# Performance work log

Hardware: AMD Instinct MI355X
Metric: run time of the kernel (lower is better)

## Reference

```python
import jax, jax.numpy as jnp
import numpy as np

GROUPS = 8

def conv1d(x, w, b, stride=1, groups=1):
    # x: [B,C,L], w: [O, I//groups, K]
    y = jax.lax.conv_general_dilated(x, w, (stride,), 'VALID',
        dimension_numbers=('NCH', 'OIH', 'NCH'), feature_group_count=groups)
    return y + b[None, :, None]

def shuffle1d(x, groups):
    B, C, L = x.shape
    cpg = C // groups
    return x.reshape(B, groups, cpg, L).transpose(0, 2, 1, 3).reshape(B, C, L)

def setup_inputs() -> dict:
    key = jax.random.key(0)
    ks = jax.random.split(key, 12)
    C = 256
    B, L = 8, 4096
    g = GROUPS
    sc = 0.05
    inp = {
        'x':   jax.random.normal(ks[0], (B, C, L), dtype=jnp.float32),
        'w1':  jax.random.normal(ks[1], (C, C // g, 3), dtype=jnp.float32) * sc,
        'b1':  jax.random.normal(ks[2], (C,), dtype=jnp.float32) * sc,
        'w2':  jax.random.normal(ks[3], (C, C // g, 3), dtype=jnp.float32) * sc,
        'b2':  jax.random.normal(ks[4], (C,), dtype=jnp.float32) * sc,
        'wa1': jax.random.normal(ks[5], (C, 2 * C // g, 1), dtype=jnp.float32) * sc,
        'ba1': jax.random.normal(ks[6], (C,), dtype=jnp.float32) * sc,
        'wa2': jax.random.normal(ks[7], (C, C // g, 1), dtype=jnp.float32) * sc,
        'ba2': jax.random.normal(ks[8], (C,), dtype=jnp.float32) * sc,
        'w3':  jax.random.normal(ks[9], (C, C // g, 5), dtype=jnp.float32) * sc,  # kernel_size-4=5
        'b3':  jax.random.normal(ks[10], (C,), dtype=jnp.float32) * sc,
    }
    return inp

def reference(x, w1, b1, w2, b2, wa1, ba1, wa2, ba2, w3, b3):
    g = GROUPS
    # in_state has length 0 at init, so cat is identity; L >= kernel_size.
    h = conv1d(x, w1, b1, stride=1, groups=g)      # [B,C,L-2]
    h = shuffle1d(h, g)
    h = conv1d(h, w2, b2, stride=1, groups=g)      # [B,C,L-4]
    h = shuffle1d(h, g)
    # SortAttn: stable ascending sort over channel dim
    sorted_h = jnp.sort(h, axis=1, stable=True)
    a = conv1d(jnp.concatenate((sorted_h, h), axis=1), wa1, ba1, stride=1, groups=g)
    a = shuffle1d(a, g)
    a = jax.nn.sigmoid(conv1d(a, wa2, ba2, stride=1, groups=g))
    h = h * a
    y = conv1d(h, w3, b3, stride=1, groups=g)      # [B,C,L-8]
    return y
```

## Files before the change

### kernel.cpp

```cpp
#include <hip/hip_runtime.h>
#include <math.h>

#define BB 8
#define CCH 256
#define LLEN 4096
#define L1V 4094
#define L2V 4092
#define L3V 4088
#define NCOL (BB * L2V)

__global__ void prep_kernel(const float* __restrict__ wa1, const float* __restrict__ wa2,
                            float* __restrict__ wt1T, float* __restrict__ wt2T) {
    int i = blockIdx.x;
    int o = threadIdx.x;
    if (i < 64) {
        wt1T[i * 256 + o] = wa1[o * 64 + i];
    } else {
        int ii = i - 64;
        if (ii < 32) wt2T[ii * 256 + o] = wa2[o * 32 + ii];
    }
}

__global__ __launch_bounds__(256, 4) void conv1_kernel(const float* __restrict__ x,
                                                       const float* __restrict__ w1,
                                                       const float* __restrict__ b1,
                                                       float* __restrict__ t1) {
    __shared__ float xs[9248];
    const int b = blockIdx.y;
    const int l0 = blockIdx.x * 32;
    const int t = threadIdx.x;

#pragma unroll
    for (int j = 0; j < 9; ++j) {
        int f = t + 256 * j;
        int row = f / 9;
        int q = f - row * 9;
        size_t rb = (size_t)(b * CCH + row) * LLEN;
        float4 v;
        int base = l0 + 4 * q;
        if (base + 3 < LLEN) {
            v = *(const float4*)(x + rb + base);
        } else {
            v.x = x[rb + min(base + 0, LLEN - 1)];
            v.y = x[rb + min(base + 1, LLEN - 1)];
            v.z = x[rb + min(base + 2, LLEN - 1)];
            v.w = x[rb + min(base + 3, LLEN - 1)];
        }
        int a = row * 36 + (row >> 5) * 4 + 4 * q;
        *(float4*)&xs[a] = v;
    }
    __syncthreads();

    const int oc = t;
    const int go = t >> 5;
    float acc[32];
#pragma unroll
    for (int l = 0; l < 32; ++l) acc[l] = 0.f;

    for (int i = 0; i < 32; ++i) {
        int row = go * 32 + i;
        int base = row * 36 + go * 4;
        float wv0 = w1[oc * 96 + i * 3 + 0];
        float wv1 = w1[oc * 96 + i * 3 + 1];
        float wv2 = w1[oc * 96 + i * 3 + 2];
#pragma unroll
        for (int q = 0; q < 9; ++q) {
            float4 v = *(const float4*)&xs[base + 4 * q];
#pragma unroll
            for (int j = 0; j < 4; ++j) {
                int e = 4 * q + j;
                float xv = (&v.x)[j];
                if (e < 32) acc[e] += wv0 * xv;
                if (e >= 1 && e <= 32) acc[e - 1] += wv1 * xv;
                if (e >= 2 && e <= 33) acc[e - 2] += wv2 * xv;
            }
        }
    }
    float bias = b1[oc];
    int nc = (oc & 31) * 8 + (oc >> 5);
    float* dst = t1 + (size_t)(b * L1V + l0) * CCH + nc;
#pragma unroll
    for (int l = 0; l < 32; ++l) {
        if (l0 + l < L1V) dst[(size_t)l * CCH] = acc[l] + bias;
    }
}

__global__ __launch_bounds__(256, 4) void conv2_kernel(const float* __restrict__ t1,
                                                       const float* __restrict__ w2,
                                                       const float* __restrict__ b2,
                                                       float* __restrict__ t2) {
    __shared__ float ts[9792];
    const int b = blockIdx.y;
    const int l0 = blockIdx.x * 32;
    const int t = threadIdx.x;

#pragma unroll
    for (int j = 0; j < 9; ++j) {
        int f = t + 256 * j;
        if (f < 2176) {
            int p = f >> 6;
            int c4 = (f & 63) * 4;
            int row = min(l0 + p, L1V - 1);
            float4 v = *(const float4*)(t1 + (size_t)(b * L1V + row) * CCH + c4);
            *(float4*)&ts[p * 288 + (c4 >> 5) * 36 + (c4 & 31)] = v;
        }
    }
    __syncthreads();

    const int oc = t;
    const int go = t >> 5;
    float acc[32];
#pragma unroll
    for (int l = 0; l < 32; ++l) acc[l] = 0.f;

    for (int i4 = 0; i4 < 8; ++i4) {
        float wv[12];
#pragma unroll
        for (int z = 0; z < 12; ++z) wv[z] = w2[oc * 96 + i4 * 12 + z];
        int colbase = go * 36 + i4 * 4;
#pragma unroll
        for (int p = 0; p < 34; ++p) {
            float4 rv = *(const float4*)&ts[p * 288 + colbase];
#pragma unroll
            for (int cc = 0; cc < 4; ++cc) {
                float xv = (&rv.x)[cc];
#pragma unroll
                for (int k = 0; k < 3; ++k) {
                    int l = p - k;
                    if (l >= 0 && l < 32) acc[l] += wv[cc * 3 + k] * xv;
                }
            }
        }
    }
    float bias = b2[oc];
    int nc = (oc & 31) * 8 + (oc >> 5);
    float* dst = t2 + (size_t)(b * L2V + l0) * CCH + nc;
#pragma unroll
    for (int l = 0; l < 32; ++l) {
        if (l0 + l < L2V) dst[(size_t)l * CCH] = acc[l] + bias;
    }
}

__device__ __forceinline__ void ce_pair(float& a, float& b, bool up) {
    float lo = fminf(a, b), hi = fmaxf(a, b);
    a = up ? lo : hi;
    b = up ? hi : lo;
}

__device__ __forceinline__ void bitonic256(float v[4], int lane) {
#pragma unroll
    for (int k = 2; k <= 256; k <<= 1) {
#pragma unroll
        for (int j = k >> 1; j > 0; j >>= 1) {
            if (j >= 4) {
                int lm = j >> 2;
                bool upper = (lane & lm) != 0;
#pragma unroll
                for (int r = 0; r < 4; ++r) {
                    float other = __shfl_xor(v[r], lm, 64);
                    bool dirUp = (((4 * lane + r) & k) == 0);
                    bool keepMin = (dirUp != upper);
                    float lo = fminf(v[r], other), hi = fmaxf(v[r], other);
                    v[r] = keepMin ? lo : hi;
                }
            } else if (j == 2) {
#pragma unroll
                for (int r = 0; r < 2; ++r) {
                    bool up = (((4 * lane + r) & k) == 0);
                    ce_pair(v[r], v[r + 2], up);
                }
            } else {
#pragma unroll
                for (int r = 0; r < 4; r += 2) {
                    bool up = (((4 * lane + r) & k) == 0);
                    ce_pair(v[r], v[r + 1], up);
                }
            }
        }
    }
}

__global__ __launch_bounds__(256, 4) void attn_kernel(float* __restrict__ t2,
                                                      const float* __restrict__ wt1T,
                                                      const float* __restrict__ wt2T,
                                                      const float* __restrict__ ba1,
                                                      const float* __restrict__ ba2) {
    __shared__ float sm[8320];
    const int t = threadIdx.x;
    const int wv = t >> 6;
    const int lane = t & 63;
    const int wbase = wv * 2080;
    const int go = lane >> 3;

    float4 ba1v = *(const float4*)&ba1[4 * lane];
    float4 ba2v = *(const float4*)&ba2[4 * lane];

    const int colBase = blockIdx.x * 16 + wv * 4;

    float4 hv[4];
#pragma unroll
    for (int cc = 0; cc < 4; ++cc) {
        hv[cc] = *(const float4*)(t2 + (size_t)(colBase + cc) * CCH + 4 * lane);
    }
#pragma unroll
    for (int r = 0; r < 4; ++r) {
        int e = 4 * lane + r;
        int slot = ((e >> 6) + 4) * 65 + (e & 63);
        float4 vvv = make_float4((&hv[0].x)[r], (&hv[1].x)[r], (&hv[2].x)[r], (&hv[3].x)[r]);
        *(float4*)&sm[wbase + slot * 4] = vvv;
    }
    float srt[4][4];
#pragma unroll
    for (int cc = 0; cc < 4; ++cc) {
        float s[4] = {hv[cc].x, hv[cc].y, hv[cc].z, hv[cc].w};
        bitonic256(s, lane);
        srt[cc][0] = s[0]; srt[cc][1] = s[1]; srt[cc][2] = s[2]; srt[cc][3] = s[3];
    }
#pragma unroll
    for (int r = 0; r < 4; ++r) {
        int e = 4 * lane + r;
        int slot = (e >> 6) * 65 + (e & 63);
        float4 vvv = make_float4(srt[0][r], srt[1][r], srt[2][r], srt[3][r]);
        *(float4*)&sm[wbase + slot * 4] = vvv;
    }

    float4 acc[4];
#pragma unroll
    for (int cc = 0; cc < 4; ++cc) acc[cc] = make_float4(0.f, 0.f, 0.f, 0.f);
#pragma unroll 4
    for (int i = 0; i < 64; ++i) {
        float4 w4 = *(const float4*)&wt1T[i * 256 + 4 * lane];
        float4 cv = *(const float4*)&sm[wbase + (go * 65 + i) * 4];
#pragma unroll
        for (int cc = 0; cc < 4; ++cc) {
            float cvv = (&cv.x)[cc];
            acc[cc].x += w4.x * cvv;
            acc[cc].y += w4.y * cvv;
            acc[cc].z += w4.z * cvv;
            acc[cc].w += w4.w * cvv;
        }
    }
#pragma unroll
    for (int r = 0; r < 4; ++r) {
        float bb = (&ba1v.x)[r];
        float4 vvv = make_float4((&acc[0].x)[r] + bb, (&acc[1].x)[r] + bb,
                                 (&acc[2].x)[r] + bb, (&acc[3].x)[r] + bb);
        *(float4*)&sm[wbase + (5 * lane + r) * 4] = vvv;
    }

    float4 acc2[4];
#pragma unroll
    for (int cc = 0; cc < 4; ++cc) acc2[cc] = make_float4(0.f, 0.f, 0.f, 0.f);
#pragma unroll 4
    for (int i = 0; i < 32; ++i) {
        float4 w4 = *(const float4*)&wt2T[i * 256 + 4 * lane];
        int idx = ((i & 7) << 5) + (go << 2) + (i >> 3);
        int slotA = idx + (idx >> 2);
        float4 av = *(const float4*)&sm[wbase + slotA * 4];
#pragma unroll
        for (int cc = 0; cc < 4; ++cc) {
            float avv = (&av.x)[cc];
            acc2[cc].x += w4.x * avv;
            acc2[cc].y += w4.y * avv;
            acc2[cc].z += w4.z * avv;
            acc2[cc].w += w4.w * avv;
        }
    }
#pragma unroll
    for (int cc = 0; cc < 4; ++cc) {
        float zx = acc2[cc].x + ba2v.x;
        float zy = acc2[cc].y + ba2v.y;
        float zz = acc2[cc].z + ba2v.z;
        float zw = acc2[cc].w + ba2v.w;
        float4 res;
        res.x = hv[cc].x * (1.f / (1.f + __expf(-zx)));
        res.y = hv[cc].y * (1.f / (1.f + __expf(-zy)));
        res.z = hv[cc].z * (1.f / (1.f + __expf(-zz)));
        res.w = hv[cc].w * (1.f / (1.f + __expf(-zw)));
        *(float4*)(t2 + (size_t)(colBase + cc) * CCH + 4 * lane) = res;
    }
}

__global__ __launch_bounds__(256, 4) void conv3_kernel(const float* __restrict__ hm,
                                                       const float* __restrict__ w3,
                                                       const float* __restrict__ b3,
                                                       float* __restrict__ out) {
    __shared__ float ts[10368];
    const int b = blockIdx.y;
    const int l0 = blockIdx.x * 32;
    const int t = threadIdx.x;

#pragma unroll
    for (int j = 0; j < 9; ++j) {
        int f = t + 256 * j;
        int p = f >> 6;
        int c4 = (f & 63) * 4;
        int row = min(l0 + p, L2V - 1);
        float4 v = *(const float4*)(hm + (size_t)(b * L2V + row) * CCH + c4);
        *(float4*)&ts[p * 288 + (c4 >> 5) * 36 + (c4 & 31)] = v;
    }
    __syncthreads();

    const int oc = t;
    const int go = t >> 5;
    float acc[32];
#pragma unroll
    for (int l = 0; l < 32; ++l) acc[l] = 0.f;

    for (int i4 = 0; i4 < 8; ++i4) {
        float wv[20];
#pragma unroll
        for (int z = 0; z < 20; ++z) wv[z] = w3[oc * 160 + i4 * 20 + z];
        int colbase = go * 36 + i4 * 4;
#pragma unroll
        for (int p = 0; p < 36; ++p) {
            float4 rv = *(const float4*)&ts[p * 288 + colbase];
#pragma unroll
            for (int cc = 0; cc < 4; ++cc) {
                float xv = (&rv.x)[cc];
#pragma unroll
                for (int k = 0; k < 5; ++k) {
                    int l = p - k;
                    if (l >= 0 && l < 32) acc[l] += wv[cc * 5 + k] * xv;
                }
            }
        }
    }
    float bias = b3[oc];
    float* dst = out + (size_t)(b * CCH + oc) * L3V + l0;
#pragma unroll
    for (int l4 = 0; l4 < 8; ++l4) {
        int gl = l0 + 4 * l4;
        if (gl + 3 < L3V) {
            float4 v;
            v.x = acc[4 * l4 + 0] + bias;
            v.y = acc[4 * l4 + 1] + bias;
            v.z = acc[4 * l4 + 2] + bias;
            v.w = acc[4 * l4 + 3] + bias;
            *(float4*)(dst + 4 * l4) = v;
        } else {
#pragma unroll
            for (int c = 0; c < 4; ++c) {
                if (gl + c < L3V) dst[4 * l4 + c] = acc[4 * l4 + c] + bias;
            }
        }
    }
}

extern "C" void kernel_launch(void* const* d_in, const int* in_sizes, int n_in,
                              void* d_out, int out_size, void* d_ws, size_t ws_size,
                              hipStream_t stream) {
    const float* x   = (const float*)d_in[0];
    const float* w1  = (const float*)d_in[1];
    const float* b1  = (const float*)d_in[2];
    const float* w2  = (const float*)d_in[3];
    const float* b2  = (const float*)d_in[4];
    const float* wa1 = (const float*)d_in[5];
    const float* ba1 = (const float*)d_in[6];
    const float* wa2 = (const float*)d_in[7];
    const float* ba2 = (const float*)d_in[8];
    const float* w3  = (const float*)d_in[9];
    const float* b3  = (const float*)d_in[10];
    float* out = (float*)d_out;

    char* ws = (char*)d_ws;
    float* t1   = (float*)ws;
    float* t2   = (float*)(ws + ((size_t)32 << 20));
    float* wt1T = (float*)(ws + ((size_t)64 << 20));
    float* wt2T = wt1T + 64 * 256;

    hipLaunchKernelGGL(prep_kernel, dim3(96), dim3(256), 0, stream, wa1, wa2, wt1T, wt2T);
    hipLaunchKernelGGL(conv1_kernel, dim3(128, BB), dim3(256), 0, stream, x, w1, b1, t1);
    hipLaunchKernelGGL(conv2_kernel, dim3(128, BB), dim3(256), 0, stream, t1, w2, b2, t2);
    hipLaunchKernelGGL(attn_kernel, dim3(2046), dim3(256), 0, stream, t2, wt1T, wt2T, ba1, ba2);
    hipLaunchKernelGGL(conv3_kernel, dim3(128, BB), dim3(256), 0, stream, t2, w3, b3, out);
}
```

Before: 303.2 us.

## Transpose conv weights, interleave bitonic sorts with swizzles, XOR-swizzle attn smem

The prep kernel now also transposes w1, w2 and w3 so that the per-output-channel weight loads in the three conv kernels are coalesced across threads instead of strided. The attention kernel's bitonic sort is rewritten as compile-time templates that sort all four columns together, using ds_swizzle for intra-32 lane exchanges and interleaving the independent columns for ILP. Its shared-memory padding is replaced by an XOR swizzle, which shrinks LDS and raises launch bounds to 5 blocks. This risks more register pressure from sorting 16 values at once under the tighter occupancy bound.

```diff
diff --git a/kernel.cpp b/kernel.cpp
--- a/kernel.cpp
+++ b/kernel.cpp
@@ -10,19 +10,28 @@
 #define NCOL (BB * L2V)
 
 __global__ void prep_kernel(const float* __restrict__ wa1, const float* __restrict__ wa2,
-                            float* __restrict__ wt1T, float* __restrict__ wt2T) {
-    int i = blockIdx.x;
+                            const float* __restrict__ w1, const float* __restrict__ w2,
+                            const float* __restrict__ w3,
+                            float* __restrict__ wt1T, float* __restrict__ wt2T,
+                            float* __restrict__ w1T, float* __restrict__ w2T,
+                            float* __restrict__ w3T) {
+    int r = blockIdx.x;
     int o = threadIdx.x;
-    if (i < 64) {
-        wt1T[i * 256 + o] = wa1[o * 64 + i];
+    if (r < 64) {
+        wt1T[r * 256 + o] = wa1[o * 64 + r];
+    } else if (r < 96) {
+        wt2T[(r - 64) * 256 + o] = wa2[o * 32 + (r - 64)];
+    } else if (r < 192) {
+        w1T[(r - 96) * 256 + o] = w1[o * 96 + (r - 96)];
+    } else if (r < 288) {
+        w2T[(r - 192) * 256 + o] = w2[o * 96 + (r - 192)];
     } else {
-        int ii = i - 64;
-        if (ii < 32) wt2T[ii * 256 + o] = wa2[o * 32 + ii];
+        w3T[(r - 288) * 256 + o] = w3[o * 160 + (r - 288)];
     }
 }
 
 __global__ __launch_bounds__(256, 4) void conv1_kernel(const float* __restrict__ x,
-                                                       const float* __restrict__ w1,
+                                                       const float* __restrict__ w1T,
                                                        const float* __restrict__ b1,
                                                        float* __restrict__ t1) {
     __shared__ float xs[9248];
@@ -60,9 +69,9 @@
     for (int i = 0; i < 32; ++i) {
         int row = go * 32 + i;
         int base = row * 36 + go * 4;
-        float wv0 = w1[oc * 96 + i * 3 + 0];
-        float wv1 = w1[oc * 96 + i * 3 + 1];
-        float wv2 = w1[oc * 96 + i * 3 + 2];
+        float wv0 = w1T[(i * 3 + 0) * 256 + oc];
+        float wv1 = w1T[(i * 3 + 1) * 256 + oc];
+        float wv2 = w1T[(i * 3 + 2) * 256 + oc];
 #pragma unroll
         for (int q = 0; q < 9; ++q) {
             float4 v = *(const float4*)&xs[base + 4 * q];
@@ -86,7 +95,7 @@
 }
 
 __global__ __launch_bounds__(256, 4) void conv2_kernel(const float* __restrict__ t1,
-                                                       const float* __restrict__ w2,
+                                                       const float* __restrict__ w2T,
                                                        const float* __restrict__ b2,
                                                        float* __restrict__ t2) {
     __shared__ float ts[9792];
@@ -116,7 +125,7 @@
     for (int i4 = 0; i4 < 8; ++i4) {
         float wv[12];
 #pragma unroll
-        for (int z = 0; z < 12; ++z) wv[z] = w2[oc * 96 + i4 * 12 + z];
+        for (int z = 0; z < 12; ++z) wv[z] = w2T[(i4 * 12 + z) * 256 + oc];
         int colbase = go * 36 + i4 * 4;
 #pragma unroll
         for (int p = 0; p < 34; ++p) {
@@ -147,49 +156,63 @@
     b = up ? hi : lo;
 }
 
-__device__ __forceinline__ void bitonic256(float v[4], int lane) {
-#pragma unroll
-    for (int k = 2; k <= 256; k <<= 1) {
-#pragma unroll
-        for (int j = k >> 1; j > 0; j >>= 1) {
-            if (j >= 4) {
-                int lm = j >> 2;
-                bool upper = (lane & lm) != 0;
-#pragma unroll
-                for (int r = 0; r < 4; ++r) {
-                    float other = __shfl_xor(v[r], lm, 64);
-                    bool dirUp = (((4 * lane + r) & k) == 0);
-                    bool keepMin = (dirUp != upper);
-                    float lo = fminf(v[r], other), hi = fmaxf(v[r], other);
-                    v[r] = keepMin ? lo : hi;
-                }
-            } else if (j == 2) {
-#pragma unroll
-                for (int r = 0; r < 2; ++r) {
-                    bool up = (((4 * lane + r) & k) == 0);
-                    ce_pair(v[r], v[r + 2], up);
-                }
-            } else {
-#pragma unroll
-                for (int r = 0; r < 4; r += 2) {
-                    bool up = (((4 * lane + r) & k) == 0);
-                    ce_pair(v[r], v[r + 1], up);
-                }
+template<int LM>
+__device__ __forceinline__ float swz(float x) {
+    return __int_as_float(__builtin_amdgcn_ds_swizzle(__float_as_int(x), (LM << 10) | 0x1F));
+}
+
+template<int K, int J>
+__device__ __forceinline__ void mstep(float v[4][4], int lane) {
+    if constexpr (J >= 4) {
+        constexpr int LM = J >> 2;
+        const bool upper = (lane & LM) != 0;
+#pragma unroll
+        for (int r = 0; r < 4; ++r) {
+            const bool dirUp = (((4 * lane + r) & K) == 0);
+            const bool keepMin = (dirUp != upper);
+#pragma unroll
+            for (int c = 0; c < 4; ++c) {
+                float other;
+                if constexpr (LM == 32) other = __shfl_xor(v[c][r], 32, 64);
+                else other = swz<LM>(v[c][r]);
+                float lo = fminf(v[c][r], other), hi = fmaxf(v[c][r], other);
+                v[c][r] = keepMin ? lo : hi;
             }
         }
-    }
-}
-
-__global__ __launch_bounds__(256, 4) void attn_kernel(float* __restrict__ t2,
+    } else if constexpr (J == 2) {
+#pragma unroll
+        for (int r = 0; r < 2; ++r) {
+            const bool up = (((4 * lane + r) & K) == 0);
+#pragma unroll
+            for (int c = 0; c < 4; ++c) ce_pair(v[c][r], v[c][r + 2], up);
+        }
+    } else {
+#pragma unroll
+        for (int r = 0; r < 4; r += 2) {
+            const bool up = (((4 * lane + r) & K) == 0);
+#pragma unroll
+            for (int c = 0; c < 4; ++c) ce_pair(v[c][r], v[c][r + 1], up);
+        }
+    }
+    if constexpr (J > 1) mstep<K, (J >> 1)>(v, lane);
+}
+
+template<int K>
+__device__ __forceinline__ void msort(float v[4][4], int lane) {
+    mstep<K, (K >> 1)>(v, lane);
+    if constexpr (K < 256) msort<(K << 1)>(v, lane);
+}
+
+__global__ __launch_bounds__(256, 5) void attn_kernel(float* __restrict__ t2,
                                                       const float* __restrict__ wt1T,
                                                       const float* __restrict__ wt2T,
                                                       const float* __restrict__ ba1,
                                                       const float* __restrict__ ba2) {
-    __shared__ float sm[8320];
+    __shared__ float sm[8192];
     const int t = threadIdx.x;
     const int wv = t >> 6;
     const int lane = t & 63;
-    const int wbase = wv * 2080;
+    const int wbase = wv << 11;
     const int go = lane >> 3;
 
     float4 ba1v = *(const float4*)&ba1[4 * lane];
@@ -205,22 +228,24 @@
 #pragma unroll
     for (int r = 0; r < 4; ++r) {
         int e = 4 * lane + r;
-        int slot = ((e >> 6) + 4) * 65 + (e & 63);
+        int ch = (e >> 6) + 4;
+        int slot = ch * 64 + ((e & 63) ^ ch);
         float4 vvv = make_float4((&hv[0].x)[r], (&hv[1].x)[r], (&hv[2].x)[r], (&hv[3].x)[r]);
         *(float4*)&sm[wbase + slot * 4] = vvv;
     }
-    float srt[4][4];
-#pragma unroll
-    for (int cc = 0; cc < 4; ++cc) {
-        float s[4] = {hv[cc].x, hv[cc].y, hv[cc].z, hv[cc].w};
-        bitonic256(s, lane);
-        srt[cc][0] = s[0]; srt[cc][1] = s[1]; srt[cc][2] = s[2]; srt[cc][3] = s[3];
-    }
+    float v[4][4];
+#pragma unroll
+    for (int cc = 0; cc < 4; ++cc)
+#pragma unroll
+        for (int r = 0; r < 4; ++r) v[cc][r] = (&hv[cc].x)[r];
+    msort<2>(v, lane);
+
 #pragma unroll
     for (int r = 0; r < 4; ++r) {
         int e = 4 * lane + r;
-        int slot = (e >> 6) * 65 + (e & 63);
-        float4 vvv = make_float4(srt[0][r], srt[1][r], srt[2][r], srt[3][r]);
+        int ch = e >> 6;
+        int slot = ch * 64 + ((e & 63) ^ ch);
+        float4 vvv = make_float4(v[0][r], v[1][r], v[2][r], v[3][r]);
         *(float4*)&sm[wbase + slot * 4] = vvv;
     }
 
@@ -230,7 +255,7 @@
 #pragma unroll 4
     for (int i = 0; i < 64; ++i) {
         float4 w4 = *(const float4*)&wt1T[i * 256 + 4 * lane];
-        float4 cv = *(const float4*)&sm[wbase + (go * 65 + i) * 4];
+        float4 cv = *(const float4*)&sm[wbase + (go * 64 + (i ^ go)) * 4];
 #pragma unroll
         for (int cc = 0; cc < 4; ++cc) {
             float cvv = (&cv.x)[cc];
@@ -282,7 +307,7 @@
 }
 
 __global__ __launch_bounds__(256, 4) void conv3_kernel(const float* __restrict__ hm,
-                                                       const float* __restrict__ w3,
+                                                       const float* __restrict__ w3T,
                                                        const float* __restrict__ b3,
                                                        float* __restrict__ out) {
     __shared__ float ts[10368];
@@ -310,7 +335,7 @@
     for (int i4 = 0; i4 < 8; ++i4) {
         float wv[20];
 #pragma unroll
-        for (int z = 0; z < 20; ++z) wv[z] = w3[oc * 160 + i4 * 20 + z];
+        for (int z = 0; z < 20; ++z) wv[z] = w3T[(i4 * 20 + z) * 256 + oc];
         int colbase = go * 36 + i4 * 4;
 #pragma unroll
         for (int p = 0; p < 36; ++p) {
@@ -368,10 +393,14 @@
     float* t2   = (float*)(ws + ((size_t)32 << 20));
     float* wt1T = (float*)(ws + ((size_t)64 << 20));
     float* wt2T = wt1T + 64 * 256;
-
-    hipLaunchKernelGGL(prep_kernel, dim3(96), dim3(256), 0, stream, wa1, wa2, wt1T, wt2T);
-    hipLaunchKernelGGL(conv1_kernel, dim3(128, BB), dim3(256), 0, stream, x, w1, b1, t1);
-    hipLaunchKernelGGL(conv2_kernel, dim3(128, BB), dim3(256), 0, stream, t1, w2, b2, t2);
+    float* w1T  = wt2T + 32 * 256;
+    float* w2T  = w1T + 96 * 256;
+    float* w3T  = w2T + 96 * 256;
+
+    hipLaunchKernelGGL(prep_kernel, dim3(448), dim3(256), 0, stream,
+                       wa1, wa2, w1, w2, w3, wt1T, wt2T, w1T, w2T, w3T);
+    hipLaunchKernelGGL(conv1_kernel, dim3(128, BB), dim3(256), 0, stream, x, w1T, b1, t1);
+    hipLaunchKernelGGL(conv2_kernel, dim3(128, BB), dim3(256), 0, stream, t1, w2T, b2, t2);
     hipLaunchKernelGGL(attn_kernel, dim3(2046), dim3(256), 0, stream, t2, wt1T, wt2T, ba1, ba2);
-    hipLaunchKernelGGL(conv3_kernel, dim3(128, BB), dim3(256), 0, stream, t2, w3, b3, out);
-}
+    hipLaunchKernelGGL(conv3_kernel, dim3(128, BB), dim3(256), 0, stream, t2, w3T, b3, out);
+}
```

Result: faster. 282.2 us (median of 2 runs) (-6.9%).
